# Kernel optimization log

Hardware: AMD Instinct MI355X
Metric: run time of the kernel (lower is better)

The kernel has to match this reference:

```python
import jax, jax.numpy as jnp
import numpy as np

N_NODES = 100000


def sage_conv(x, src, dst, Wl, bl, Wr):
    # PyG SAGEConv (aggr='mean'): out = lin_l(mean_{j in N(i)} x_j) + lin_r(x_i)
    msg = x[src]                                                   # [E, d] gather
    agg = jax.ops.segment_sum(msg, dst, num_segments=N_NODES)      # [N, d]
    cnt = jax.ops.segment_sum(jnp.ones((src.shape[0], 1), x.dtype), dst,
                              num_segments=N_NODES)                # [N, 1]
    mean = agg / jnp.maximum(cnt, 1.0)
    return mean @ Wl + bl + x @ Wr


def setup_inputs() -> dict:
    key = jax.random.key(0)
    ks = jax.random.split(key, 9)
    N, E, D_IN = N_NODES, 3200000, 64
    x = jax.random.normal(ks[0], (N, D_IN), dtype=jnp.float32)
    edge_index = jax.random.randint(ks[1], (2, E), 0, N, dtype=jnp.int64)

    def glorot(k, fan_in, fan_out):
        lim = float(np.sqrt(6.0 / (fan_in + fan_out)))
        return jax.random.uniform(k, (fan_in, fan_out), jnp.float32, -lim, lim)

    return {
        "x": x,
        "edge_index": edge_index,
        "W1l": glorot(ks[2], D_IN, 64), "b1": jnp.zeros((64,), jnp.float32),
        "W1r": glorot(ks[3], D_IN, 64),
        "W2l": glorot(ks[4], 64, 32), "b2": jnp.zeros((32,), jnp.float32),
        "W2r": glorot(ks[5], 64, 32),
        "W3l": glorot(ks[6], 32, 1), "b3": jnp.zeros((1,), jnp.float32),
        "W3r": glorot(ks[7], 32, 1),
    }


def reference(x, edge_index, W1l, b1, W1r, W2l, b2, W2r, W3l, b3, W3r):
    src, dst = edge_index[0], edge_index[1]
    h = jax.nn.relu(sage_conv(x, src, dst, W1l, b1, W1r))   # dropout: eval mode (identity)
    h = jax.nn.relu(sage_conv(h, src, dst, W2l, b2, W2r))
    h = sage_conv(h, src, dst, W3l, b3, W3r)
    return jax.nn.sigmoid(h)                                # [N, 1]
```

## Files before the change

### kernel.cpp

```cpp
#include <hip/hip_runtime.h>
#include <math.h>

#define NN 100000
#define NB 391
#define BT 8192
#define CAP 12288

typedef float vfloat2 __attribute__((ext_vector_type(2)));
typedef short short8 __attribute__((ext_vector_type(8)));
typedef float floatx4 __attribute__((ext_vector_type(4)));

__device__ __forceinline__ unsigned short f2bf(float f) {
    unsigned int u = __float_as_uint(f);
    u += 0x7fffu + ((u >> 16) & 1u);
    return (unsigned short)(u >> 16);
}

__device__ __forceinline__ unsigned char f2fp8(float f) {
    const int p = __builtin_amdgcn_cvt_pk_fp8_f32(f, f, 0, false);
    return (unsigned char)(p & 0xFF);
}
template <bool HI>
__device__ __forceinline__ vfloat2 fp8pk2(unsigned int w) {
    return __builtin_amdgcn_cvt_pk_f32_fp8((int)w, HI);
}

template <int D_IN, int CL, int CR, int NPB, int FUSE_IN>
__global__ void __launch_bounds__(256)
mlp_mfma_kernel(const float* __restrict__ in0,
                const float* __restrict__ in1,
                const float* __restrict__ Wl,
                const float* __restrict__ Wr,
                const float* __restrict__ bias,
                unsigned char* __restrict__ yout,
                float* __restrict__ zout,
                int n_nodes) {
    constexpr int COLS = CL + CR;
    constexpr int CT = COLS / 16;
    constexpr int KT = D_IN / 32;
    constexpr int NT = NPB / 16;
    constexpr int KG = D_IN / 8;
    __shared__ short sA[NT * KT * 64 * 8];
    __shared__ short sB[CT * KT * 64 * 8];
    __shared__ float sBias[CR];
    const int t = threadIdx.x;
    const int node0 = blockIdx.x * NPB;

    for (int i = t; i < NPB * KG; i += 256) {
        const int nl = i / KG, kg = i % KG;
        const int n = node0 + nl;
        float v[8];
        if (n < n_nodes) {
            const float4* p = (const float4*)(in0 + (long long)n * D_IN + kg * 8);
            float4 a0 = p[0], a1 = p[1];
            if (FUSE_IN) {
                const float4* q = (const float4*)(in1 + (long long)n * D_IN + kg * 8);
                const float4 b0 = q[0], b1 = q[1];
                a0.x = fmaxf(a0.x + b0.x, 0.f); a0.y = fmaxf(a0.y + b0.y, 0.f);
                a0.z = fmaxf(a0.z + b0.z, 0.f); a0.w = fmaxf(a0.w + b0.w, 0.f);
                a1.x = fmaxf(a1.x + b1.x, 0.f); a1.y = fmaxf(a1.y + b1.y, 0.f);
                a1.z = fmaxf(a1.z + b1.z, 0.f); a1.w = fmaxf(a1.w + b1.w, 0.f);
            }
            v[0] = a0.x; v[1] = a0.y; v[2] = a0.z; v[3] = a0.w;
            v[4] = a1.x; v[5] = a1.y; v[6] = a1.z; v[7] = a1.w;
        } else {
#pragma unroll
            for (int j = 0; j < 8; ++j) v[j] = 0.f;
        }
        short8 s;
#pragma unroll
        for (int j = 0; j < 8; ++j) s[j] = (short)f2bf(v[j]);
        const int nt = nl >> 4, m = nl & 15, kt = kg >> 2, quad = kg & 3;
        ((short8*)sA)[(nt * KT + kt) * 64 + quad * 16 + m] = s;
    }
    for (int i = t; i < CT * KT * 64; i += 256) {
        const int ct = i / (KT * 64);
        const int rem = i % (KT * 64);
        const int kt = rem / 64, L = rem % 64;
        const int c = ct * 16 + (L & 15);
        const int k0 = kt * 32 + (L >> 4) * 8;
        short8 s;
#pragma unroll
        for (int j = 0; j < 8; ++j) {
            const int k = k0 + j;
            const float w = (c < CL) ? Wl[k * CL + c] : Wr[k * CR + (c - CL)];
            s[j] = (short)f2bf(w);
        }
        ((short8*)sB)[i] = s;
    }
    for (int i = t; i < CR; i += 256) sBias[i] = bias[i];
    __syncthreads();

    const int w = t >> 6, lane = t & 63;
    short8 Bf[CT][KT];
#pragma unroll
    for (int ct = 0; ct < CT; ++ct)
#pragma unroll
        for (int kt = 0; kt < KT; ++kt)
            Bf[ct][kt] = ((short8*)sB)[(ct * KT + kt) * 64 + lane];
    const int col = lane & 15, quad = lane >> 4;
#pragma unroll
    for (int nti = 0; nti < NT / 4; ++nti) {
        const int nt = w * (NT / 4) + nti;
        short8 A[KT];
#pragma unroll
        for (int kt = 0; kt < KT; ++kt)
            A[kt] = ((short8*)sA)[(nt * KT + kt) * 64 + lane];
        const int nodeb = node0 + nt * 16 + quad * 4;
#pragma unroll
        for (int ct = 0; ct < CT; ++ct) {
            floatx4 acc = {0.f, 0.f, 0.f, 0.f};
#pragma unroll
            for (int kt = 0; kt < KT; ++kt)
                acc = __builtin_amdgcn_mfma_f32_16x16x32_bf16(A[kt], Bf[ct][kt], acc, 0, 0, 0);
            const int gc = ct * 16 + col;
#pragma unroll
            for (int r = 0; r < 4; ++r) {
                const int node = nodeb + r;
                if (node < n_nodes) {
                    if (gc < CL) yout[(long long)node * CL + gc] = f2fp8(acc[r]);
                    else zout[(long long)node * CR + (gc - CL)] = acc[r] + sBias[gc - CL];
                }
            }
        }
    }
}

template <int D_IN>
__global__ void __launch_bounds__(256)
mlp3_kernel(const float* __restrict__ mean,
            const float* __restrict__ z,
            const float* __restrict__ W3l,
            const float* __restrict__ W3r,
            const float* __restrict__ b3,
            float* __restrict__ y,
            float* __restrict__ z3, int n_nodes) {
    __shared__ float swl[D_IN], swr[D_IN];
    const int t = threadIdx.x;
    if (t < D_IN) { swl[t] = W3l[t]; swr[t] = W3r[t]; }
    __syncthreads();
    const int n = blockIdx.x * 256 + t;
    if (n >= n_nodes) return;
    const float4* pm = (const float4*)(mean + (long long)n * D_IN);
    const float4* pz = (const float4*)(z + (long long)n * D_IN);
    float accl = 0.f, accr = 0.f;
#pragma unroll
    for (int q = 0; q < D_IN / 4; ++q) {
        const float4 m4 = pm[q];
        const float4 z4 = pz[q];
        const float h0 = fmaxf(m4.x + z4.x, 0.f);
        const float h1 = fmaxf(m4.y + z4.y, 0.f);
        const float h2 = fmaxf(m4.z + z4.z, 0.f);
        const float h3 = fmaxf(m4.w + z4.w, 0.f);
        accl += h0 * swl[4 * q] + h1 * swl[4 * q + 1] + h2 * swl[4 * q + 2] + h3 * swl[4 * q + 3];
        accr += h0 * swr[4 * q] + h1 * swr[4 * q + 1] + h2 * swr[4 * q + 2] + h3 * swr[4 * q + 3];
    }
    y[n] = accl;
    z3[n] = accr + b3[0];
}

__global__ void bucket_hist_kernel(const int* __restrict__ dst,
                                   int* __restrict__ bcnt, int n_edges) {
    __shared__ int lh[NB];
    for (int i = threadIdx.x; i < NB; i += 256) lh[i] = 0;
    __syncthreads();
    const int stride = gridDim.x * 256;
    for (int i = blockIdx.x * 256 + threadIdx.x; i < n_edges; i += stride)
        atomicAdd(&lh[dst[i] >> 8], 1);
    __syncthreads();
    for (int i = threadIdx.x; i < NB; i += 256)
        if (lh[i]) atomicAdd(&bcnt[i], lh[i]);
}

__global__ void __launch_bounds__(512)
bucket_scan_kernel(const int* __restrict__ bcnt, int* __restrict__ boffs,
                   int* __restrict__ bcursor) {
    __shared__ int s[512];
    const int t = threadIdx.x;
    const int v = (t < NB) ? bcnt[t] : 0;
    s[t] = v;
    __syncthreads();
    for (int off = 1; off < 512; off <<= 1) {
        const int tmp = (t >= off) ? s[t - off] : 0;
        __syncthreads();
        s[t] += tmp;
        __syncthreads();
    }
    const int excl = s[t] - v;
    if (t <= NB) boffs[t] = excl;
    if (t < NB) bcursor[t] = excl;
}

__global__ void __launch_bounds__(512)
bin_edges_kernel(const int* __restrict__ src, const int* __restrict__ dst,
                 int* __restrict__ bcursor, unsigned int* __restrict__ binned,
                 int n_edges) {
    __shared__ unsigned int stage[BT];
    __shared__ unsigned short sbkt[BT];
    __shared__ int lhist[512], lscan[512], lstart[512], gbase[512], lcur[512];
    const int t = threadIdx.x;
    const int e0 = blockIdx.x * BT;
    const int count = min(BT, n_edges - e0);
    lhist[t] = 0;
    __syncthreads();
    for (int i = t; i < count; i += 512) atomicAdd(&lhist[dst[e0 + i] >> 8], 1);
    __syncthreads();
    const int v = lhist[t];
    lscan[t] = v;
    __syncthreads();
    for (int off = 1; off < 512; off <<= 1) {
        const int tmp = (t >= off) ? lscan[t - off] : 0;
        __syncthreads();
        lscan[t] += tmp;
        __syncthreads();
    }
    const int excl = lscan[t] - v;
    lstart[t] = excl;
    lcur[t] = excl;
    if (t < NB && v > 0) gbase[t] = atomicAdd(&bcursor[t], v);
    __syncthreads();
    for (int i = t; i < count; i += 512) {
        const int d = dst[e0 + i];
        const int b = d >> 8;
        const int p = atomicAdd(&lcur[b], 1);
        stage[p] = (unsigned int)src[e0 + i] | ((unsigned int)(d & 255) << 17);
        sbkt[p] = (unsigned short)b;
    }
    __syncthreads();
    for (int i = t; i < count; i += 512) {
        const int b = sbkt[i];
        binned[gbase[b] + (i - lstart[b])] = stage[i];
    }
}

__global__ void __launch_bounds__(1024)
csr_sort_kernel(const unsigned int* __restrict__ binned,
                const int* __restrict__ boffs,
                int* __restrict__ ssrc, int* __restrict__ row_ptr,
                float* __restrict__ inv_deg, int n_nodes, int n_edges) {
    __shared__ int stage[CAP];
    __shared__ int hist[256];
    __shared__ int lexcl[256];
    __shared__ int lcur[256];
    const int t = threadIdx.x;
    const int b = blockIdx.x;
    const int s0 = boffs[b], s1 = boffs[b + 1];
    const int count = s1 - s0;
    if (t < 256) hist[t] = 0;
    __syncthreads();
    for (int i = t; i < count; i += 1024)
        atomicAdd(&hist[binned[s0 + i] >> 17], 1);
    __syncthreads();
    if (t < 256) lexcl[t] = hist[t];
    __syncthreads();
    for (int off = 1; off < 256; off <<= 1) {
        int tmp = 0;
        if (t < 256 && t >= off) tmp = lexcl[t - off];
        __syncthreads();
        if (t < 256) lexcl[t] += tmp;
        __syncthreads();
    }
    if (t < 256) {
        const int excl = lexcl[t] - hist[t];
        lcur[t] = excl;
        const int n = (b << 8) + t;
        if (n < n_nodes) {
            row_ptr[n] = s0 + excl;
            inv_deg[n] = 1.0f / (float)max(hist[t], 1);
        }
    }
    if (b == NB - 1 && t == 0) row_ptr[n_nodes] = n_edges;
    __syncthreads();
    for (int i = t; i < count; i += 1024) {
        const unsigned int v = binned[s0 + i];
        const int p = atomicAdd(&lcur[v >> 17], 1);
        if (p < CAP) stage[p] = (int)(v & 0x1FFFFu);
    }
    __syncthreads();
    for (int i = t; i < count; i += 1024) ssrc[s0 + i] = stage[i];
}

template <int D, int EP>
__global__ void __launch_bounds__(256)
agg_mean_fp8_kernel(const unsigned int* __restrict__ yb,
                    const int* __restrict__ row_ptr,
                    const int* __restrict__ ssrc,
                    const float* __restrict__ inv_deg,
                    float* __restrict__ mean, int n_nodes) {
    constexpr int G = D / 16;
    constexpr int TPN = EP * G;
    constexpr int NPB = 256 / TPN;
    const int t = threadIdx.x;
    const int g = t / TPN;
    const int sub = t % TPN;
    const int lane = sub % G;
    const int team = sub / G;
    const int n = blockIdx.x * NPB + g;
    if (n >= n_nodes) return;
    const int s0 = row_ptr[n], s1 = row_ptr[n + 1];
    const int cnt = s1 - s0;
    const int b0 = s0 + (cnt * team) / EP;
    const int b1 = s0 + (cnt * (team + 1)) / EP;
    const uint4* yv = (const uint4*)yb;
    float acc[16];
#pragma unroll
    for (int i = 0; i < 16; ++i) acc[i] = 0.f;
    int e = b0;
    for (; e + 4 <= b1; e += 4) {
        int sidx[4];
#pragma unroll
        for (int q = 0; q < 4; ++q) sidx[q] = __builtin_nontemporal_load(ssrc + e + q);
        uint4 v[4];
#pragma unroll
        for (int q = 0; q < 4; ++q) v[q] = yv[(long long)sidx[q] * G + lane];
#pragma unroll
        for (int q = 0; q < 4; ++q) {
            const unsigned int wx = v[q].x, wy = v[q].y, wz = v[q].z, ww = v[q].w;
            vfloat2 p;
            p = fp8pk2<false>(wx); acc[0]  += p.x; acc[1]  += p.y;
            p = fp8pk2<true>(wx);  acc[2]  += p.x; acc[3]  += p.y;
            p = fp8pk2<false>(wy); acc[4]  += p.x; acc[5]  += p.y;
            p = fp8pk2<true>(wy);  acc[6]  += p.x; acc[7]  += p.y;
            p = fp8pk2<false>(wz); acc[8]  += p.x; acc[9]  += p.y;
            p = fp8pk2<true>(wz);  acc[10] += p.x; acc[11] += p.y;
            p = fp8pk2<false>(ww); acc[12] += p.x; acc[13] += p.y;
            p = fp8pk2<true>(ww);  acc[14] += p.x; acc[15] += p.y;
        }
    }
    for (; e < b1; ++e) {
        const int si = __builtin_nontemporal_load(ssrc + e);
        const uint4 v = yv[(long long)si * G + lane];
        vfloat2 p;
        p = fp8pk2<false>(v.x); acc[0]  += p.x; acc[1]  += p.y;
        p = fp8pk2<true>(v.x);  acc[2]  += p.x; acc[3]  += p.y;
        p = fp8pk2<false>(v.y); acc[4]  += p.x; acc[5]  += p.y;
        p = fp8pk2<true>(v.y);  acc[6]  += p.x; acc[7]  += p.y;
        p = fp8pk2<false>(v.z); acc[8]  += p.x; acc[9]  += p.y;
        p = fp8pk2<true>(v.z);  acc[10] += p.x; acc[11] += p.y;
        p = fp8pk2<false>(v.w); acc[12] += p.x; acc[13] += p.y;
        p = fp8pk2<true>(v.w);  acc[14] += p.x; acc[15] += p.y;
    }
#pragma unroll
    for (int o = G; o < TPN; o <<= 1)
#pragma unroll
        for (int i = 0; i < 16; ++i) acc[i] += __shfl_xor(acc[i], o, 64);
    if (team == 0) {
        const float inv = inv_deg[n];
        floatx4* mv = (floatx4*)mean + (long long)n * (D / 4) + lane * 4;
#pragma unroll
        for (int q = 0; q < 4; ++q) {
            floatx4 o = {acc[4 * q] * inv, acc[4 * q + 1] * inv,
                         acc[4 * q + 2] * inv, acc[4 * q + 3] * inv};
            __builtin_nontemporal_store(o, mv + q);
        }
    }
}

__global__ void agg_mean_d1_sig_kernel(const float* __restrict__ y,
                                       const int* __restrict__ row_ptr,
                                       const int* __restrict__ ssrc,
                                       const float* __restrict__ inv_deg,
                                       const float* __restrict__ z3,
                                       float* __restrict__ out, int n_nodes) {
    const int wave = threadIdx.x >> 6;
    const int lane = threadIdx.x & 63;
    const int n = blockIdx.x * 4 + wave;
    if (n >= n_nodes) return;
    const int s0 = row_ptr[n], s1 = row_ptr[n + 1];
    float acc = 0.f;
    for (int e = s0 + lane; e < s1; e += 64)
        acc += y[__builtin_nontemporal_load(ssrc + e)];
    for (int off = 32; off > 0; off >>= 1) acc += __shfl_down(acc, off, 64);
    if (lane == 0) out[n] = 1.0f / (1.0f + expf(-(acc * inv_deg[n] + z3[n])));
}

extern "C" void kernel_launch(void* const* d_in, const int* in_sizes, int n_in,
                              void* d_out, int out_size, void* d_ws, size_t ws_size,
                              hipStream_t stream) {
    const float* x = (const float*)d_in[0];
    const int* edge_index = (const int*)d_in[1];
    const float* W1l = (const float*)d_in[2];
    const float* b1  = (const float*)d_in[3];
    const float* W1r = (const float*)d_in[4];
    const float* W2l = (const float*)d_in[5];
    const float* b2  = (const float*)d_in[6];
    const float* W2r = (const float*)d_in[7];
    const float* W3l = (const float*)d_in[8];
    const float* b3  = (const float*)d_in[9];
    const float* W3r = (const float*)d_in[10];
    float* out = (float*)d_out;

    const int E = in_sizes[1] / 2;
    const int* src = edge_index;
    const int* dst = edge_index + E;

    float* bufY    = (float*)d_ws;
    float* meanB   = bufY + 32LL * NN;
    float* z1      = meanB + 64LL * NN;
    float* z2      = z1 + 64LL * NN;
    float* z3      = z2 + 32LL * NN;
    float* inv_deg = z3 + NN;
    int* bcnt      = (int*)(inv_deg + NN);
    int* boffs     = bcnt + NB;
    int* bcursor   = boffs + NB + 1;
    int* row_ptr   = bcursor + NB;
    int* ssrc      = row_ptr + NN + 1;
    unsigned int* binned = (unsigned int*)z1;

    const int ntiles = (E + BT - 1) / BT;

    (void)hipMemsetAsync(bcnt, 0, NB * sizeof(int), stream);
    bucket_hist_kernel<<<512, 256, 0, stream>>>(dst, bcnt, E);
    bucket_scan_kernel<<<1, 512, 0, stream>>>(bcnt, boffs, bcursor);
    bin_edges_kernel<<<ntiles, 512, 0, stream>>>(src, dst, bcursor, binned, E);
    csr_sort_kernel<<<NB, 1024, 0, stream>>>(binned, boffs, ssrc, row_ptr, inv_deg, NN, E);

    mlp_mfma_kernel<64, 64, 64, 128, 0><<<(NN + 127) / 128, 256, 0, stream>>>(
        x, nullptr, W1l, W1r, b1, (unsigned char*)bufY, z1, NN);
    agg_mean_fp8_kernel<64, 2><<<(NN + 31) / 32, 256, 0, stream>>>(
        (const unsigned int*)bufY, row_ptr, ssrc, inv_deg, meanB, NN);

    mlp_mfma_kernel<64, 32, 32, 128, 1><<<(NN + 127) / 128, 256, 0, stream>>>(
        meanB, z1, W2l, W2r, b2, (unsigned char*)bufY, z2, NN);
    agg_mean_fp8_kernel<32, 4><<<(NN + 31) / 32, 256, 0, stream>>>(
        (const unsigned int*)bufY, row_ptr, ssrc, inv_deg, meanB, NN);

    mlp3_kernel<32><<<(NN + 255) / 256, 256, 0, stream>>>(
        meanB, z2, W3l, W3r, b3, bufY, z3, NN);
    agg_mean_d1_sig_kernel<<<(NN + 3) / 4, 256, 0, stream>>>(
        bufY, row_ptr, ssrc, inv_deg, z3, out, NN);
}
```

Measured before the change: 301.5 us.

## Split neighbor aggregation into two source-half passes for cache locality

The CSR sort now orders each node's edges by whether the source index falls in the lower or upper half of the nodes, and records a per-node midpoint. Each fp8 mean aggregation becomes two kernel launches, one gathering from each half of the feature table. The aim is to shrink each pass's gather working set so it stays cache-resident. The cost is an extra launch, writing and re-reading partial sums to the mean buffer, and a larger sort histogram.

```diff
diff --git a/kernel.cpp b/kernel.cpp
--- a/kernel.cpp
+++ b/kernel.cpp
@@ -5,6 +5,7 @@
 #define NB 391
 #define BT 8192
 #define CAP 12288
+#define SRC_HALF 50000
 
 typedef float vfloat2 __attribute__((ext_vector_type(2)));
 typedef short short8 __attribute__((ext_vector_type(8)));
@@ -237,56 +238,65 @@
 csr_sort_kernel(const unsigned int* __restrict__ binned,
                 const int* __restrict__ boffs,
                 int* __restrict__ ssrc, int* __restrict__ row_ptr,
-                float* __restrict__ inv_deg, int n_nodes, int n_edges) {
+                int* __restrict__ rowmid, float* __restrict__ inv_deg,
+                int n_nodes, int n_edges) {
     __shared__ int stage[CAP];
-    __shared__ int hist[256];
-    __shared__ int lexcl[256];
-    __shared__ int lcur[256];
+    __shared__ int hist[512];
+    __shared__ int lincl[512];
+    __shared__ int lcur[512];
     const int t = threadIdx.x;
     const int b = blockIdx.x;
     const int s0 = boffs[b], s1 = boffs[b + 1];
     const int count = s1 - s0;
-    if (t < 256) hist[t] = 0;
-    __syncthreads();
-    for (int i = t; i < count; i += 1024)
-        atomicAdd(&hist[binned[s0 + i] >> 17], 1);
-    __syncthreads();
-    if (t < 256) lexcl[t] = hist[t];
-    __syncthreads();
-    for (int off = 1; off < 256; off <<= 1) {
+    if (t < 512) hist[t] = 0;
+    __syncthreads();
+    for (int i = t; i < count; i += 1024) {
+        const unsigned int v = binned[s0 + i];
+        const int key = (int)((v >> 17) << 1) | ((v & 0x1FFFFu) >= SRC_HALF ? 1 : 0);
+        atomicAdd(&hist[key], 1);
+    }
+    __syncthreads();
+    if (t < 512) lincl[t] = hist[t];
+    __syncthreads();
+    for (int off = 1; off < 512; off <<= 1) {
         int tmp = 0;
-        if (t < 256 && t >= off) tmp = lexcl[t - off];
-        __syncthreads();
-        if (t < 256) lexcl[t] += tmp;
-        __syncthreads();
-    }
+        if (t < 512 && t >= off) tmp = lincl[t - off];
+        __syncthreads();
+        if (t < 512) lincl[t] += tmp;
+        __syncthreads();
+    }
+    if (t < 512) lcur[t] = lincl[t] - hist[t];
     if (t < 256) {
-        const int excl = lexcl[t] - hist[t];
-        lcur[t] = excl;
+        const int S = lincl[2 * t] - hist[2 * t];
+        const int M = lincl[2 * t];
+        const int En = lincl[2 * t + 1];
         const int n = (b << 8) + t;
         if (n < n_nodes) {
-            row_ptr[n] = s0 + excl;
-            inv_deg[n] = 1.0f / (float)max(hist[t], 1);
+            row_ptr[n] = s0 + S;
+            rowmid[n] = s0 + M;
+            inv_deg[n] = 1.0f / (float)max(En - S, 1);
         }
     }
     if (b == NB - 1 && t == 0) row_ptr[n_nodes] = n_edges;
     __syncthreads();
     for (int i = t; i < count; i += 1024) {
         const unsigned int v = binned[s0 + i];
-        const int p = atomicAdd(&lcur[v >> 17], 1);
+        const int key = (int)((v >> 17) << 1) | ((v & 0x1FFFFu) >= SRC_HALF ? 1 : 0);
+        const int p = atomicAdd(&lcur[key], 1);
         if (p < CAP) stage[p] = (int)(v & 0x1FFFFu);
     }
     __syncthreads();
     for (int i = t; i < count; i += 1024) ssrc[s0 + i] = stage[i];
 }
 
-template <int D, int EP>
+template <int D, int EP, int PHASE>
 __global__ void __launch_bounds__(256)
-agg_mean_fp8_kernel(const unsigned int* __restrict__ yb,
-                    const int* __restrict__ row_ptr,
-                    const int* __restrict__ ssrc,
-                    const float* __restrict__ inv_deg,
-                    float* __restrict__ mean, int n_nodes) {
+agg_mean_fp8_phase_kernel(const unsigned int* __restrict__ yb,
+                          const int* __restrict__ row_ptr,
+                          const int* __restrict__ rowmid,
+                          const int* __restrict__ ssrc,
+                          const float* __restrict__ inv_deg,
+                          float* __restrict__ mean, int n_nodes) {
     constexpr int G = D / 16;
     constexpr int TPN = EP * G;
     constexpr int NPB = 256 / TPN;
@@ -297,7 +307,9 @@
     const int team = sub / G;
     const int n = blockIdx.x * NPB + g;
     if (n >= n_nodes) return;
-    const int s0 = row_ptr[n], s1 = row_ptr[n + 1];
+    int s0, s1;
+    if (PHASE == 0) { s0 = row_ptr[n]; s1 = rowmid[n]; }
+    else            { s0 = rowmid[n];  s1 = row_ptr[n + 1]; }
     const int cnt = s1 - s0;
     const int b0 = s0 + (cnt * team) / EP;
     const int b1 = s0 + (cnt * (team + 1)) / EP;
@@ -345,13 +357,22 @@
 #pragma unroll
         for (int i = 0; i < 16; ++i) acc[i] += __shfl_xor(acc[i], o, 64);
     if (team == 0) {
-        const float inv = inv_deg[n];
         floatx4* mv = (floatx4*)mean + (long long)n * (D / 4) + lane * 4;
-#pragma unroll
-        for (int q = 0; q < 4; ++q) {
-            floatx4 o = {acc[4 * q] * inv, acc[4 * q + 1] * inv,
-                         acc[4 * q + 2] * inv, acc[4 * q + 3] * inv};
-            __builtin_nontemporal_store(o, mv + q);
+        if (PHASE == 0) {
+#pragma unroll
+            for (int q = 0; q < 4; ++q) {
+                floatx4 o = {acc[4 * q], acc[4 * q + 1], acc[4 * q + 2], acc[4 * q + 3]};
+                __builtin_nontemporal_store(o, mv + q);
+            }
+        } else {
+            const float inv = inv_deg[n];
+#pragma unroll
+            for (int q = 0; q < 4; ++q) {
+                const floatx4 pr = __builtin_nontemporal_load(mv + q);
+                floatx4 o = {(acc[4 * q] + pr.x) * inv, (acc[4 * q + 1] + pr.y) * inv,
+                             (acc[4 * q + 2] + pr.z) * inv, (acc[4 * q + 3] + pr.w) * inv};
+                __builtin_nontemporal_store(o, mv + q);
+            }
         }
     }
 }
@@ -405,6 +426,7 @@
     int* bcursor   = boffs + NB + 1;
     int* row_ptr   = bcursor + NB;
     int* ssrc      = row_ptr + NN + 1;
+    int* rowmid    = ssrc + E;
     unsigned int* binned = (unsigned int*)z1;
 
     const int ntiles = (E + BT - 1) / BT;
@@ -413,17 +435,22 @@
     bucket_hist_kernel<<<512, 256, 0, stream>>>(dst, bcnt, E);
     bucket_scan_kernel<<<1, 512, 0, stream>>>(bcnt, boffs, bcursor);
     bin_edges_kernel<<<ntiles, 512, 0, stream>>>(src, dst, bcursor, binned, E);
-    csr_sort_kernel<<<NB, 1024, 0, stream>>>(binned, boffs, ssrc, row_ptr, inv_deg, NN, E);
+    csr_sort_kernel<<<NB, 1024, 0, stream>>>(binned, boffs, ssrc, row_ptr, rowmid,
+                                             inv_deg, NN, E);
 
     mlp_mfma_kernel<64, 64, 64, 128, 0><<<(NN + 127) / 128, 256, 0, stream>>>(
         x, nullptr, W1l, W1r, b1, (unsigned char*)bufY, z1, NN);
-    agg_mean_fp8_kernel<64, 2><<<(NN + 31) / 32, 256, 0, stream>>>(
-        (const unsigned int*)bufY, row_ptr, ssrc, inv_deg, meanB, NN);
+    agg_mean_fp8_phase_kernel<64, 2, 0><<<(NN + 31) / 32, 256, 0, stream>>>(
+        (const unsigned int*)bufY, row_ptr, rowmid, ssrc, inv_deg, meanB, NN);
+    agg_mean_fp8_phase_kernel<64, 2, 1><<<(NN + 31) / 32, 256, 0, stream>>>(
+        (const unsigned int*)bufY, row_ptr, rowmid, ssrc, inv_deg, meanB, NN);
 
     mlp_mfma_kernel<64, 32, 32, 128, 1><<<(NN + 127) / 128, 256, 0, stream>>>(
         meanB, z1, W2l, W2r, b2, (unsigned char*)bufY, z2, NN);
-    agg_mean_fp8_kernel<32, 4><<<(NN + 31) / 32, 256, 0, stream>>>(
-        (const unsigned int*)bufY, row_ptr, ssrc, inv_deg, meanB, NN);
+    agg_mean_fp8_phase_kernel<32, 4, 0><<<(NN + 31) / 32, 256, 0, stream>>>(
+        (const unsigned int*)bufY, row_ptr, rowmid, ssrc, inv_deg, meanB, NN);
+    agg_mean_fp8_phase_kernel<32, 4, 1><<<(NN + 31) / 32, 256, 0, stream>>>(
+        (const unsigned int*)bufY, row_ptr, rowmid, ssrc, inv_deg, meanB, NN);
 
     mlp3_kernel<32><<<(NN + 255) / 256, 256, 0, stream>>>(
         meanB, z2, W3l, W3r, b3, bufY, z3, NN);
```

New measurement: 337.9 us. 12.1% more time.

## Sub-sort CSR neighbors by source range and drop split-edge aggregation teams

Applied to the files above, without the earlier changes.

The CSR sort now buckets each destination's edges into four source-id ranges, so neighbor lists are partly ordered by source index. The intent is better cache locality for the feature gathers during aggregation. The aggregation kernel also drops the multi-team edge split and shuffle reduction, so one group of G threads handles a whole node and each block covers more nodes. The sort prefix scan grows from 256 to 1024 entries, and per-node load balance across teams is lost.

```diff
diff --git a/kernel.cpp b/kernel.cpp
--- a/kernel.cpp
+++ b/kernel.cpp
@@ -5,6 +5,7 @@
 #define NB 391
 #define BT 8192
 #define CAP 12288
+#define SRC_Q 25000
 
 typedef float vfloat2 __attribute__((ext_vector_type(2)));
 typedef short short8 __attribute__((ext_vector_type(8)));
@@ -239,48 +240,52 @@
                 int* __restrict__ ssrc, int* __restrict__ row_ptr,
                 float* __restrict__ inv_deg, int n_nodes, int n_edges) {
     __shared__ int stage[CAP];
-    __shared__ int hist[256];
-    __shared__ int lexcl[256];
-    __shared__ int lcur[256];
+    __shared__ int hist[1024];
+    __shared__ int lincl[1024];
+    __shared__ int lcur[1024];
     const int t = threadIdx.x;
     const int b = blockIdx.x;
     const int s0 = boffs[b], s1 = boffs[b + 1];
     const int count = s1 - s0;
-    if (t < 256) hist[t] = 0;
-    __syncthreads();
-    for (int i = t; i < count; i += 1024)
-        atomicAdd(&hist[binned[s0 + i] >> 17], 1);
-    __syncthreads();
-    if (t < 256) lexcl[t] = hist[t];
-    __syncthreads();
-    for (int off = 1; off < 256; off <<= 1) {
-        int tmp = 0;
-        if (t < 256 && t >= off) tmp = lexcl[t - off];
-        __syncthreads();
-        if (t < 256) lexcl[t] += tmp;
-        __syncthreads();
-    }
+    hist[t] = 0;
+    __syncthreads();
+    for (int i = t; i < count; i += 1024) {
+        const unsigned int v = binned[s0 + i];
+        const int key = (int)((v >> 17) << 2) | ((int)(v & 0x1FFFFu) / SRC_Q);
+        atomicAdd(&hist[key], 1);
+    }
+    __syncthreads();
+    lincl[t] = hist[t];
+    __syncthreads();
+    for (int off = 1; off < 1024; off <<= 1) {
+        const int tmp = (t >= off) ? lincl[t - off] : 0;
+        __syncthreads();
+        lincl[t] += tmp;
+        __syncthreads();
+    }
+    lcur[t] = lincl[t] - hist[t];
     if (t < 256) {
-        const int excl = lexcl[t] - hist[t];
-        lcur[t] = excl;
+        const int S = lincl[4 * t] - hist[4 * t];
+        const int En = lincl[4 * t + 3];
         const int n = (b << 8) + t;
         if (n < n_nodes) {
-            row_ptr[n] = s0 + excl;
-            inv_deg[n] = 1.0f / (float)max(hist[t], 1);
+            row_ptr[n] = s0 + S;
+            inv_deg[n] = 1.0f / (float)max(En - S, 1);
         }
     }
     if (b == NB - 1 && t == 0) row_ptr[n_nodes] = n_edges;
     __syncthreads();
     for (int i = t; i < count; i += 1024) {
         const unsigned int v = binned[s0 + i];
-        const int p = atomicAdd(&lcur[v >> 17], 1);
+        const int key = (int)((v >> 17) << 2) | ((int)(v & 0x1FFFFu) / SRC_Q);
+        const int p = atomicAdd(&lcur[key], 1);
         if (p < CAP) stage[p] = (int)(v & 0x1FFFFu);
     }
     __syncthreads();
     for (int i = t; i < count; i += 1024) ssrc[s0 + i] = stage[i];
 }
 
-template <int D, int EP>
+template <int D>
 __global__ void __launch_bounds__(256)
 agg_mean_fp8_kernel(const unsigned int* __restrict__ yb,
                     const int* __restrict__ row_ptr,
@@ -288,25 +293,18 @@
                     const float* __restrict__ inv_deg,
                     float* __restrict__ mean, int n_nodes) {
     constexpr int G = D / 16;
-    constexpr int TPN = EP * G;
-    constexpr int NPB = 256 / TPN;
-    const int t = threadIdx.x;
-    const int g = t / TPN;
-    const int sub = t % TPN;
-    const int lane = sub % G;
-    const int team = sub / G;
+    constexpr int NPB = 256 / G;
+    const int g = threadIdx.x / G;
+    const int lane = threadIdx.x % G;
     const int n = blockIdx.x * NPB + g;
     if (n >= n_nodes) return;
     const int s0 = row_ptr[n], s1 = row_ptr[n + 1];
-    const int cnt = s1 - s0;
-    const int b0 = s0 + (cnt * team) / EP;
-    const int b1 = s0 + (cnt * (team + 1)) / EP;
     const uint4* yv = (const uint4*)yb;
     float acc[16];
 #pragma unroll
     for (int i = 0; i < 16; ++i) acc[i] = 0.f;
-    int e = b0;
-    for (; e + 4 <= b1; e += 4) {
+    int e = s0;
+    for (; e + 4 <= s1; e += 4) {
         int sidx[4];
 #pragma unroll
         for (int q = 0; q < 4; ++q) sidx[q] = __builtin_nontemporal_load(ssrc + e + q);
@@ -327,7 +325,7 @@
             p = fp8pk2<true>(ww);  acc[14] += p.x; acc[15] += p.y;
         }
     }
-    for (; e < b1; ++e) {
+    for (; e < s1; ++e) {
         const int si = __builtin_nontemporal_load(ssrc + e);
         const uint4 v = yv[(long long)si * G + lane];
         vfloat2 p;
@@ -340,19 +338,13 @@
         p = fp8pk2<false>(v.w); acc[12] += p.x; acc[13] += p.y;
         p = fp8pk2<true>(v.w);  acc[14] += p.x; acc[15] += p.y;
     }
-#pragma unroll
-    for (int o = G; o < TPN; o <<= 1)
-#pragma unroll
-        for (int i = 0; i < 16; ++i) acc[i] += __shfl_xor(acc[i], o, 64);
-    if (team == 0) {
-        const float inv = inv_deg[n];
-        floatx4* mv = (floatx4*)mean + (long long)n * (D / 4) + lane * 4;
-#pragma unroll
-        for (int q = 0; q < 4; ++q) {
-            floatx4 o = {acc[4 * q] * inv, acc[4 * q + 1] * inv,
-                         acc[4 * q + 2] * inv, acc[4 * q + 3] * inv};
-            __builtin_nontemporal_store(o, mv + q);
-        }
+    const float inv = inv_deg[n];
+    floatx4* mv = (floatx4*)mean + (long long)n * (D / 4) + lane * 4;
+#pragma unroll
+    for (int q = 0; q < 4; ++q) {
+        floatx4 o = {acc[4 * q] * inv, acc[4 * q + 1] * inv,
+                     acc[4 * q + 2] * inv, acc[4 * q + 3] * inv};
+        __builtin_nontemporal_store(o, mv + q);
     }
 }
 
@@ -413,16 +405,17 @@
     bucket_hist_kernel<<<512, 256, 0, stream>>>(dst, bcnt, E);
     bucket_scan_kernel<<<1, 512, 0, stream>>>(bcnt, boffs, bcursor);
     bin_edges_kernel<<<ntiles, 512, 0, stream>>>(src, dst, bcursor, binned, E);
-    csr_sort_kernel<<<NB, 1024, 0, stream>>>(binned, boffs, ssrc, row_ptr, inv_deg, NN, E);
+    csr_sort_kernel<<<NB, 1024, 0, stream>>>(binned, boffs, ssrc, row_ptr,
+                                             inv_deg, NN, E);
 
     mlp_mfma_kernel<64, 64, 64, 128, 0><<<(NN + 127) / 128, 256, 0, stream>>>(
         x, nullptr, W1l, W1r, b1, (unsigned char*)bufY, z1, NN);
-    agg_mean_fp8_kernel<64, 2><<<(NN + 31) / 32, 256, 0, stream>>>(
+    agg_mean_fp8_kernel<64><<<(NN + 63) / 64, 256, 0, stream>>>(
         (const unsigned int*)bufY, row_ptr, ssrc, inv_deg, meanB, NN);
 
     mlp_mfma_kernel<64, 32, 32, 128, 1><<<(NN + 127) / 128, 256, 0, stream>>>(
         meanB, z1, W2l, W2r, b2, (unsigned char*)bufY, z2, NN);
-    agg_mean_fp8_kernel<32, 4><<<(NN + 31) / 32, 256, 0, stream>>>(
+    agg_mean_fp8_kernel<32><<<(NN + 127) / 128, 256, 0, stream>>>(
         (const unsigned int*)bufY, row_ptr, ssrc, inv_deg, meanB, NN);
 
     mlp3_kernel<32><<<(NN + 255) / 256, 256, 0, stream>>>(
```

After: 319.2 us. 1.06x slower.
